# Optimization experiments

Measured on AMD Instinct MI355X. Metric: run time of the kernel, lower is better.

## Reference

```python
import jax, jax.numpy as jnp
import numpy as np

RADIUS = 5.0          # cutoff radius (Angstrom)
MAX_NBR = 32          # max_num_neighbors_threshold
CELL_L = 12.0         # cubic box edge; > 2*RADIUS/2 so rep=1 (27 image cells)


def setup_inputs() -> dict:
    key = jax.random.key(0)
    k1, _ = jax.random.split(key)
    B, N = 16, 256
    pos = jax.random.uniform(k1, (B, N, 3), dtype=jnp.float32) * CELL_L
    cell = jnp.tile(jnp.eye(3, dtype=jnp.float32)[None] * CELL_L, (B, 1, 1))
    return {"pos": pos, "cell": cell}


def reference(pos, cell):
    # pos: [B,N,3] atom positions, cell: [B,3,3] lattice vectors (rows a1,a2,a3)
    B, N, _ = pos.shape
    # periodic image offsets n in {-1,0,1}^3 -> unit: [C,3], C=27
    r = jnp.arange(-1, 2, dtype=pos.dtype)
    n1, n2, n3 = jnp.meshgrid(r, r, r, indexing="ij")
    unit = jnp.stack([n1.ravel(), n2.ravel(), n3.ravel()], axis=-1)  # [C,3]
    C = unit.shape[0]
    # pbc_offsets[b,c,:] = sum_k n_k * a_k  (== bmm(cell^T, unit^T) in torch code)
    offsets = jnp.einsum("ck,bkd->bcd", unit, cell)  # [B,C,3]
    # candidate edge vectors: receiver i, source j shifted by image offset c
    dvec = pos[:, :, None, None, :] - (pos[:, None, :, None, :] + offsets[:, None, None, :, :])  # [B,N,N,C,3]
    dsqr = jnp.sum(dvec * dvec, axis=-1)  # [B,N,N,C]
    # radius mask + remove self (atom_distance_sqr > 1e-4)
    within = (dsqr <= RADIUS * RADIUS) & (dsqr > 1e-4)
    M = N * C
    dsqr_f = jnp.where(within, dsqr, jnp.inf).reshape(B, N, M)
    # per-receiver sort-based top-K truncation (mirrors get_max_neighbors_mask:
    # index_copy into [num_atoms, max_nbr] padded with inf, sort, keep first K finite)
    order = jnp.argsort(dsqr_f, axis=-1)
    rank = jnp.argsort(order, axis=-1)           # rank of each candidate among its receiver's neighbors
    keep = (rank < MAX_NBR) & jnp.isfinite(dsqr_f)  # [B,N,M] final edge mask
    dist = jnp.where(keep, jnp.sqrt(jnp.where(keep, dsqr_f, 1.0)), 0.0)  # masked edge lengths
    dvec_m = jnp.where(keep[..., None], dvec.reshape(B, N, M, 3), 0.0)   # masked edge vectors
    # num_neighbors_image == segment_csr(clamp(num_neighbors, K)) == per-image kept-edge count
    num_neighbors_image = jnp.sum(keep.reshape(B, -1), axis=-1).astype(jnp.int32)
    return dist, dvec_m, num_neighbors_image
```

## Files before the change

kernel.cpp:

```cpp
#include <hip/hip_runtime.h>
#include <stdint.h>


constexpr int B_ = 16, N_ = 256, C_ = 27;
constexpr int M_ = N_ * C_;
constexpr int MAXC = 256;
constexpr int KMAX = 32;

typedef float vfloat4 __attribute__((ext_vector_type(4)));

__device__ __forceinline__ void nt_store4(float* p, float a, float b, float c, float d) {
    vfloat4 v; v.x = a; v.y = b; v.z = c; v.w = d;
    __builtin_nontemporal_store(v, (vfloat4*)p);
}

__global__ __launch_bounds__(256)
void nbr_kernel(const float* __restrict__ pos,
                const float* __restrict__ cell,
                float* __restrict__ dist,
                float* __restrict__ dvec,
                float* __restrict__ nn)
{
#pragma clang fp contract(off)
    __shared__ float offx[C_], offy[C_], offz[C_];
    __shared__ unsigned long long keys[MAXC];
    __shared__ float4 vals[MAXC];
    __shared__ float4 kept[KMAX];
    __shared__ unsigned char slot[M_];
    __shared__ int cnt;

    const int bi  = blockIdx.x;
    const int b   = bi >> 8;
    const int i   = bi & 255;
    const int tid = threadIdx.x;

    const float* pb = pos + b * N_ * 3;
    const float pjx = pb[tid * 3 + 0], pjy = pb[tid * 3 + 1], pjz = pb[tid * 3 + 2];
    const float pix = pb[i * 3 + 0],   piy = pb[i * 3 + 1],   piz = pb[i * 3 + 2];

    if (tid < C_) {
        const float n1 = (float)(tid / 9 - 1);
        const float n2 = (float)((tid / 3) % 3 - 1);
        const float n3 = (float)(tid % 3 - 1);
        const float* cb = cell + b * 9;
        offx[tid] = n1 * cb[0] + n2 * cb[3] + n3 * cb[6];
        offy[tid] = n1 * cb[1] + n2 * cb[4] + n3 * cb[7];
        offz[tid] = n1 * cb[2] + n2 * cb[5] + n3 * cb[8];
    }
    uint32_t* slot32 = (uint32_t*)slot;
    for (int w = tid; w < M_ / 4; w += 256) slot32[w] = 0;
    if (tid == 0) cnt = 0;
    __syncthreads();

    #pragma unroll 1
    for (int c = 0; c < C_; ++c) {
        const float sx = pjx + offx[c], sy = pjy + offy[c], sz = pjz + offz[c];
        const float dx = pix - sx, dy = piy - sy, dz = piz - sz;
        const float dsq = dx * dx + dy * dy + dz * dz;
        if (dsq <= 25.0f && dsq > 1e-4f) {
            const int idx = atomicAdd(&cnt, 1);
            if (idx < MAXC) {
                keys[idx] = ((unsigned long long)__float_as_uint(dsq) << 32)
                          | (unsigned)(tid * C_ + c);
                vals[idx] = make_float4(dx, dy, dz, dsq);
            }
        }
    }
    __syncthreads();

    int K = cnt; if (K > MAXC) K = MAXC;
    if (tid == 0)
        atomicAdd(&nn[b], (float)(K < KMAX ? K : KMAX));

    for (int idx = tid; idx < K; idx += 256) {
        const unsigned long long key = keys[idx];
        int r = 0;
        for (int q = 0; q < K; ++q) r += (keys[q] < key) ? 1 : 0;
        if (r < KMAX) {
            const int m = (int)(key & 0xffffffffu);
            const float4 v = vals[idx];
            kept[r] = make_float4(v.x, v.y, v.z, sqrtf(v.w));
            slot[m] = (unsigned char)(r + 1);
        }
    }
    __syncthreads();

    float* drow = dist + (size_t)bi * M_;
    float* vrow = dvec + (size_t)bi * (size_t)(M_ * 3);

    for (int g = tid; g < M_ / 4; g += 256) {
        float o0 = 0.f, o1 = 0.f, o2 = 0.f, o3 = 0.f;
        const uint32_t s4 = slot32[g];
        if (s4) {
            uint32_t s;
            s = s4 & 0xffu;         if (s) o0 = kept[s - 1].w;
            s = (s4 >> 8) & 0xffu;  if (s) o1 = kept[s - 1].w;
            s = (s4 >> 16) & 0xffu; if (s) o2 = kept[s - 1].w;
            s = (s4 >> 24) & 0xffu; if (s) o3 = kept[s - 1].w;
        }
        nt_store4(drow + 4 * g, o0, o1, o2, o3);
    }
    for (int h = tid; h < 3 * M_ / 4; h += 256) {
        const int e0 = 4 * h;
        const int m0 = e0 / 3;
        const int m1 = (e0 + 3) / 3;
        float o[4] = {0.f, 0.f, 0.f, 0.f};
        if ((slot[m0] | slot[m1]) != 0) {
            #pragma unroll
            for (int u = 0; u < 4; ++u) {
                const int e = e0 + u;
                const int m = e / 3;
                const int d = e - 3 * m;
                const uint32_t s = slot[m];
                if (s) o[u] = (&kept[s - 1].x)[d];
            }
        }
        nt_store4(vrow + e0, o[0], o[1], o[2], o[3]);
    }
}

extern "C" void kernel_launch(void* const* d_in, const int* in_sizes, int n_in,
                              void* d_out, int out_size, void* d_ws, size_t ws_size,
                              hipStream_t stream)
{
    const float* pos  = (const float*)d_in[0];
    const float* cell = (const float*)d_in[1];
    float* dist = (float*)d_out;
    float* dvec = dist + (size_t)B_ * N_ * M_;
    float* nn   = dvec + (size_t)B_ * N_ * M_ * 3;
    (void)hipMemsetAsync(nn, 0, B_ * sizeof(float), stream);
    nbr_kernel<<<dim3(B_ * N_), dim3(256), 0, stream>>>(pos, cell, dist, dvec, nn);
}
```

Baseline: 467.5 us.

## Split neighbor search and output sweep into two kernels via workspace

Splits the fused kernel in two. The first kernel finds neighbors and writes a per-row slot map and the kept edges to workspace. The second is a grid-stride kernel that writes the dense dist/dvec outputs as one flat streaming sweep across 2048 blocks. This separates the write-bandwidth-bound phase from the compute phase so the stores run at full occupancy, at the cost of an extra launch and a workspace round trip of about 7 MB for the slot maps.

Measured after the change: 506.2 us. +8.3%, slower.

```diff
diff --git a/kernel.cpp b/kernel.cpp
--- a/kernel.cpp
+++ b/kernel.cpp
@@ -6,6 +6,12 @@
 constexpr int M_ = N_ * C_;
 constexpr int MAXC = 256;
 constexpr int KMAX = 32;
+constexpr int NR   = B_ * N_;
+constexpr int DGPR = M_ / 4;
+constexpr int VGPR_ = 3 * M_ / 4;
+constexpr int DG = NR * DGPR;
+constexpr int NG = DG + NR * VGPR_;
+constexpr int SWEEP_BLOCKS = 2048;
 
 typedef float vfloat4 __attribute__((ext_vector_type(4)));
 
@@ -15,11 +21,11 @@
 }
 
 __global__ __launch_bounds__(256)
-void nbr_kernel(const float* __restrict__ pos,
-                const float* __restrict__ cell,
-                float* __restrict__ dist,
-                float* __restrict__ dvec,
-                float* __restrict__ nn)
+void edges_kernel(const float* __restrict__ pos,
+                  const float* __restrict__ cell,
+                  float* __restrict__ nn,
+                  uint32_t* __restrict__ sws,
+                  float4*  __restrict__ kws)
 {
 #pragma clang fp contract(off)
     __shared__ float offx[C_], offy[C_], offz[C_];
@@ -48,8 +54,9 @@
         offz[tid] = n1 * cb[2] + n2 * cb[5] + n3 * cb[8];
     }
     uint32_t* slot32 = (uint32_t*)slot;
-    for (int w = tid; w < M_ / 4; w += 256) slot32[w] = 0;
+    for (int w = tid; w < DGPR; w += 256) slot32[w] = 0;
     if (tid == 0) cnt = 0;
+    if (tid < KMAX) kept[tid] = make_float4(0.f, 0.f, 0.f, 0.f);
     __syncthreads();
 
     #pragma unroll 1
@@ -85,37 +92,54 @@
     }
     __syncthreads();
 
-    float* drow = dist + (size_t)bi * M_;
-    float* vrow = dvec + (size_t)bi * (size_t)(M_ * 3);
+    uint32_t* sw = sws + (size_t)bi * DGPR;
+    for (int w = tid; w < DGPR; w += 256) sw[w] = slot32[w];
+    if (tid < KMAX) kws[bi * KMAX + tid] = kept[tid];
+}
 
-    for (int g = tid; g < M_ / 4; g += 256) {
+__global__ __launch_bounds__(256)
+void sweep_kernel(const uint32_t* __restrict__ sws,
+                  const float4*  __restrict__ kws,
+                  float* __restrict__ out)
+{
+    const int stride = SWEEP_BLOCKS * 256;
+    for (int g = blockIdx.x * 256 + threadIdx.x; g < NG; g += stride) {
         float o0 = 0.f, o1 = 0.f, o2 = 0.f, o3 = 0.f;
-        const uint32_t s4 = slot32[g];
-        if (s4) {
-            uint32_t s;
-            s = s4 & 0xffu;         if (s) o0 = kept[s - 1].w;
-            s = (s4 >> 8) & 0xffu;  if (s) o1 = kept[s - 1].w;
-            s = (s4 >> 16) & 0xffu; if (s) o2 = kept[s - 1].w;
-            s = (s4 >> 24) & 0xffu; if (s) o3 = kept[s - 1].w;
-        }
-        nt_store4(drow + 4 * g, o0, o1, o2, o3);
-    }
-    for (int h = tid; h < 3 * M_ / 4; h += 256) {
-        const int e0 = 4 * h;
-        const int m0 = e0 / 3;
-        const int m1 = (e0 + 3) / 3;
-        float o[4] = {0.f, 0.f, 0.f, 0.f};
-        if ((slot[m0] | slot[m1]) != 0) {
-            #pragma unroll
-            for (int u = 0; u < 4; ++u) {
-                const int e = e0 + u;
-                const int m = e / 3;
-                const int d = e - 3 * m;
-                const uint32_t s = slot[m];
-                if (s) o[u] = (&kept[s - 1].x)[d];
+        if (g < DG) {
+            const uint32_t s4 = sws[g];
+            if (s4) {
+                const int bi = g / DGPR;
+                const float4* kb = kws + bi * KMAX;
+                uint32_t s;
+                s = s4 & 0xffu;         if (s) o0 = kb[s - 1].w;
+                s = (s4 >> 8) & 0xffu;  if (s) o1 = kb[s - 1].w;
+                s = (s4 >> 16) & 0xffu; if (s) o2 = kb[s - 1].w;
+                s = (s4 >> 24) & 0xffu; if (s) o3 = kb[s - 1].w;
+            }
+        } else {
+            const int h  = g - DG;
+            const int bi = h / VGPR_;
+            const int hh = h - bi * VGPR_;
+            const int e0 = 4 * hh;
+            const int m0 = e0 / 3;
+            const int m1 = (e0 + 3) / 3;
+            const unsigned char* sb = (const unsigned char*)sws + (size_t)bi * M_;
+            const uint32_t sA = sb[m0], sB = sb[m1];
+            if ((sA | sB) != 0) {
+                const float4* kb = kws + bi * KMAX;
+                float o[4] = {0.f, 0.f, 0.f, 0.f};
+                #pragma unroll
+                for (int u = 0; u < 4; ++u) {
+                    const int e = e0 + u;
+                    const int m = e / 3;
+                    const int d = e - 3 * m;
+                    const uint32_t s = (m == m0) ? sA : sB;
+                    if (s) o[u] = (&kb[s - 1].x)[d];
+                }
+                o0 = o[0]; o1 = o[1]; o2 = o[2]; o3 = o[3];
             }
         }
-        nt_store4(vrow + e0, o[0], o[1], o[2], o[3]);
+        nt_store4(out + 4 * (size_t)g, o0, o1, o2, o3);
     }
 }
 
@@ -125,9 +149,13 @@
 {
     const float* pos  = (const float*)d_in[0];
     const float* cell = (const float*)d_in[1];
-    float* dist = (float*)d_out;
-    float* dvec = dist + (size_t)B_ * N_ * M_;
-    float* nn   = dvec + (size_t)B_ * N_ * M_ * 3;
+    float* out = (float*)d_out;
+    float* nn  = out + (size_t)NR * M_ * 4;
+
+    uint32_t* sws = (uint32_t*)d_ws;
+    float4*   kws = (float4*)((char*)d_ws + (size_t)NR * DGPR * 4);
+
     (void)hipMemsetAsync(nn, 0, B_ * sizeof(float), stream);
-    nbr_kernel<<<dim3(B_ * N_), dim3(256), 0, stream>>>(pos, cell, dist, dvec, nn);
+    edges_kernel<<<dim3(NR), dim3(256), 0, stream>>>(pos, cell, nn, sws, kws);
+    sweep_kernel<<<dim3(SWEEP_BLOCKS), dim3(256), 0, stream>>>(sws, kws, out);
 }
```
